# Kernel tuning notes

Measured on AMD Instinct MI355X. Metric: run time of the kernel, lower is better.

## Reference

```python
import jax, jax.numpy as jnp
from jax import lax
import numpy as np

B, P, S, K = 16, 4096, 1024, 16   # clouds, points/cloud, fps samples/cloud (ratio 0.25), knn k
IN_F, OUT_F = 256, 512
EPS = 1e-5


def setup_inputs() -> dict:
    key = jax.random.key(0)
    k1, k2, k3 = jax.random.split(key, 3)
    features = jax.random.normal(k1, (B * P, IN_F), jnp.float32)
    positions = jax.random.normal(k2, (B * P, 3), jnp.float32)
    batch = jnp.repeat(jnp.arange(B, dtype=jnp.int32), P)
    W = jax.random.normal(k3, (IN_F, OUT_F), jnp.float32) / np.sqrt(IN_F)
    b = jnp.zeros((OUT_F,), jnp.float32)
    gamma = jnp.ones((OUT_F,), jnp.float32)
    beta = jnp.zeros((OUT_F,), jnp.float32)
    return {"features": features, "positions": positions, "batch": batch,
            "W": W, "b": b, "gamma": gamma, "beta": beta}


def _fps_local(pos):
    """Farthest point sampling on one cloud. pos: [P,3] -> [S] int32 local indices.
    Deterministic start at index 0 (torch_cluster fps with random_start disabled)."""
    def step(carry, _):
        min_d, last = carry
        d = jnp.sum((pos - pos[last]) ** 2, axis=-1)
        min_d = jnp.minimum(min_d, d)
        nxt = jnp.argmax(min_d).astype(jnp.int32)
        return (min_d, nxt), last
    init = (jnp.full((pos.shape[0],), jnp.inf, pos.dtype), jnp.int32(0))
    _, idx = lax.scan(step, init, None, length=S)
    return idx


def _knn_local(q, x):
    """K nearest neighbors of queries q [S,F] among x [P,F] (squared L2). -> [S,K] int32."""
    d = jnp.sum(q * q, -1, keepdims=True) - 2.0 * (q @ x.T) + jnp.sum(x * x, -1)
    _, idx = lax.top_k(-d, K)
    return idx


def reference(features, positions, batch, W, b, gamma, beta):
    pos_b = positions.reshape(B, P, 3)
    feat_b = features.reshape(B, P, IN_F)

    # --- FPS on positions, per cloud ---
    fps_loc = jax.vmap(_fps_local)(pos_b)                      # [B,S]
    offsets = (jnp.arange(B, dtype=jnp.int32) * P)[:, None]    # [B,1]
    fps_glob = (fps_loc + offsets).reshape(-1)                 # [B*S]

    # --- MLP: Linear -> BatchNorm1d (training batch stats, biased var) -> ReLU ---
    h = features @ W + b                                       # [N,OUT_F]
    mu = jnp.mean(h, axis=0)
    var = jnp.var(h, axis=0)
    h = jax.nn.relu(gamma * (h - mu) * lax.rsqrt(var + EPS) + beta)

    # --- brute-force KNN in feature space: queries = features[fps_indices] ---
    q = jnp.take_along_axis(feat_b, fps_loc[..., None], axis=1)   # [B,S,IN_F]
    nn_loc = jax.vmap(_knn_local)(q, feat_b)                      # [B,S,K]
    nn_glob = nn_loc + offsets[..., None]                         # [B,S,K]

    # --- scatter max-pool: each query has exactly K neighbors -> max over K ---
    nb = h[nn_glob.reshape(-1)].reshape(B, S, K, OUT_F)
    new_features = jnp.max(nb, axis=2).reshape(B * S, OUT_F)

    return new_features, positions[fps_glob], batch[fps_glob]
```

## Files before the change

kernel.cpp:

```cpp
#include <hip/hip_runtime.h>
#include <cstddef>


#define TD_B   16
#define TD_P   4096
#define TD_S   1024
#define TD_K   16
#define TD_INF 256
#define TD_OUTF 512

typedef __attribute__((ext_vector_type(8))) _Float16 half8;
typedef __attribute__((ext_vector_type(4))) float    f32x4;
typedef __attribute__((ext_vector_type(2))) float    v2f;

__device__ __forceinline__ unsigned short f2bf(float x) {
    unsigned u = __float_as_uint(x);
    unsigned r = (u + 0x7fffu + ((u >> 16) & 1u)) >> 16;
    return (unsigned short)r;
}

struct FpsSm {
    float4 p4[TD_P];
    int    sel[TD_S];
    unsigned long long kw[2][8];
};
struct GemmSm {
    float As[16 * 260];
    float Bs[16 * 128];
};
union SmU {
    FpsSm f; GemmSm g;
    char pad_[84000];
};

#define TD_DPPSTEP(k, ctl, bc)                                                          \
    {                                                                                   \
        unsigned yh_ = (unsigned)__builtin_amdgcn_update_dpp(                           \
            0, (int)(unsigned)((k) >> 32), (ctl), 0xf, 0xf, (bc));                      \
        unsigned yl_ = (unsigned)__builtin_amdgcn_update_dpp(                           \
            0, (int)(unsigned)(k), (ctl), 0xf, 0xf, (bc));                              \
        unsigned long long y_ = ((unsigned long long)yh_ << 32) | yl_;                  \
        if (y_ > (k)) (k) = y_;                                                         \
    }

__global__ __launch_bounds__(512)
void td_fused(const float* __restrict__ feat, const float* __restrict__ pos,
              const float* __restrict__ W, const float* __restrict__ bias,
              unsigned short* __restrict__ H, float* __restrict__ XX,
              int* __restrict__ FPSI, float* __restrict__ outP,
              float* __restrict__ outB) {
    __shared__ SmU sm;
    const int bx = blockIdx.x;
    const int t  = threadIdx.x;

    if (bx < 16) {
        __builtin_amdgcn_s_setprio(2);
        const int b = bx;
        const int w = t >> 6;
        v2f px[8], py[8], pz[8], md[8];
        int ni0[8], ni1[8];
        float lx = 0.0f, ly = 0.0f, lz = 0.0f;
        if (t < 256) {
#pragma unroll
            for (int j = 0; j < 8; ++j) {
                int p0 = j * 512 + t, p1 = p0 + 256;
                const float* q0 = pos + (size_t)(b * TD_P + p0) * 3;
                const float* q1 = pos + (size_t)(b * TD_P + p1) * 3;
                float x0 = q0[0], y0 = q0[1], z0 = q0[2];
                float x1 = q1[0], y1 = q1[1], z1 = q1[2];
                px[j] = (v2f){x0, x1}; py[j] = (v2f){y0, y1}; pz[j] = (v2f){z0, z1};
                sm.f.p4[p0] = make_float4(x0, y0, z0, 0.0f);
                sm.f.p4[p1] = make_float4(x1, y1, z1, 0.0f);
                md[j] = (v2f){__builtin_inff(), __builtin_inff()};
                ni0[j] = ~p0; ni1[j] = ~p1;
            }
            if (t == 0) sm.f.sel[0] = 0;
        }
        __syncthreads();
        if (t < 256) { float4 wp = sm.f.p4[0]; lx = wp.x; ly = wp.y; lz = wp.z; }
        for (int s = 0; s < TD_S - 1; ++s) {
            const int par = s & 1;
            if (t < 256) {
                double k[16];
                {
#pragma clang fp contract(off)
                    v2f l2x = (v2f){lx, lx}, l2y = (v2f){ly, ly}, l2z = (v2f){lz, lz};
#pragma unroll
                    for (int j = 0; j < 8; ++j) {
                        v2f dx = px[j] - l2x;
                        v2f dy = py[j] - l2y;
                        v2f dz = pz[j] - l2z;
                        v2f sx = dx * dx;
                        v2f sy = dy * dy;
                        v2f sz = dz * dz;
                        v2f dd = (sx + sy) + sz;
                        md[j] = __builtin_elementwise_min(md[j], dd);
                        k[2 * j]     = __hiloint2double(__float_as_int(md[j].x), ni0[j]);
                        k[2 * j + 1] = __hiloint2double(__float_as_int(md[j].y), ni1[j]);
                    }
                }
#pragma unroll
                for (int st = 8; st > 0; st >>= 1)
#pragma unroll
                    for (int i = 0; i < st; ++i) k[i] = fmax(k[i], k[i + st]);
                unsigned long long tk = (unsigned long long)__double_as_longlong(k[0]);
                TD_DPPSTEP(tk, 0x111, true)
                TD_DPPSTEP(tk, 0x112, true)
                TD_DPPSTEP(tk, 0x114, true)
                TD_DPPSTEP(tk, 0x118, true)
                TD_DPPSTEP(tk, 0x142, false)
                TD_DPPSTEP(tk, 0x143, false)
                if ((t & 63) == 63) sm.f.kw[par][w] = tk;
            }
            __syncthreads();
            if (t < 256) {
                const unsigned long long* kwp = sm.f.kw[par];
                double g01 = fmax(__longlong_as_double((long long)kwp[0]),
                                  __longlong_as_double((long long)kwp[1]));
                double g23 = fmax(__longlong_as_double((long long)kwp[2]),
                                  __longlong_as_double((long long)kwp[3]));
                double gk  = fmax(g01, g23);
                unsigned idx = ~(unsigned)__double2loint(gk);
                if (t == 0) sm.f.sel[s + 1] = (int)idx;
                float4 wp = sm.f.p4[idx];
                lx = wp.x; ly = wp.y; lz = wp.z;
            }
        }
        __syncthreads();
        for (int s = t; s < TD_S; s += 512) {
            int li = sm.f.sel[s];
            int og = b * TD_S + s;
            float4 wp = sm.f.p4[li];
            outP[og * 3 + 0] = wp.x;
            outP[og * 3 + 1] = wp.y;
            outP[og * 3 + 2] = wp.z;
            outB[og] = (float)b;
            FPSI[og] = b * TD_P + li;
        }
    } else if (bx < 16 + 1024) {
        const int gb = bx - 16;
        const int mb = gb >> 2, nb = gb & 3;
        const int tm = t >> 4, tn = t & 15;
        float acc[8][8];
#pragma unroll
        for (int i = 0; i < 8; ++i)
#pragma unroll
            for (int j = 0; j < 8; ++j) acc[i][j] = 0.0f;
        float* As = sm.g.As;
        float* Bs = sm.g.Bs;
        for (int kc = 0; kc < 16; ++kc) {
#pragma unroll
            for (int p2 = 0; p2 < 2; ++p2) {
                int f4 = t + 512 * p2;
                int r = f4 >> 2, c4 = f4 & 3;
                float4 v = *(const float4*)&feat[(size_t)(mb * 256 + r) * 256 + kc * 16 + c4 * 4];
                As[(c4 * 4 + 0) * 260 + r] = v.x;
                As[(c4 * 4 + 1) * 260 + r] = v.y;
                As[(c4 * 4 + 2) * 260 + r] = v.z;
                As[(c4 * 4 + 3) * 260 + r] = v.w;
            }
            {
                int kk = t >> 5, n4 = t & 31;
                float4 v = *(const float4*)&W[(size_t)(kc * 16 + kk) * 512 + nb * 128 + n4 * 4];
                *(float4*)&Bs[kk * 128 + n4 * 4] = v;
            }
            __syncthreads();
#pragma unroll
            for (int kk = 0; kk < 16; ++kk) {
                float4 a0 = *(float4*)&As[kk * 260 + tm * 8];
                float4 a1 = *(float4*)&As[kk * 260 + tm * 8 + 4];
                float4 b0 = *(float4*)&Bs[kk * 128 + tn * 8];
                float4 b1 = *(float4*)&Bs[kk * 128 + tn * 8 + 4];
                float av[8] = {a0.x, a0.y, a0.z, a0.w, a1.x, a1.y, a1.z, a1.w};
                float bv2[8] = {b0.x, b0.y, b0.z, b0.w, b1.x, b1.y, b1.z, b1.w};
#pragma unroll
                for (int i = 0; i < 8; ++i)
#pragma unroll
                    for (int j = 0; j < 8; ++j)
                        acc[i][j] = fmaf(av[i], bv2[j], acc[i][j]);
            }
            __syncthreads();
        }
        float4 bb0 = *(const float4*)&bias[nb * 128 + tn * 8];
        float4 bb1 = *(const float4*)&bias[nb * 128 + tn * 8 + 4];
        float bsv[8] = {bb0.x, bb0.y, bb0.z, bb0.w, bb1.x, bb1.y, bb1.z, bb1.w};
#pragma unroll
        for (int i = 0; i < 8; ++i) {
            int row = mb * 256 + tm * 8 + i;
            uint4 pk;
            pk.x = (unsigned)f2bf(acc[i][0] + bsv[0]) | ((unsigned)f2bf(acc[i][1] + bsv[1]) << 16);
            pk.y = (unsigned)f2bf(acc[i][2] + bsv[2]) | ((unsigned)f2bf(acc[i][3] + bsv[3]) << 16);
            pk.z = (unsigned)f2bf(acc[i][4] + bsv[4]) | ((unsigned)f2bf(acc[i][5] + bsv[5]) << 16);
            pk.w = (unsigned)f2bf(acc[i][6] + bsv[6]) | ((unsigned)f2bf(acc[i][7] + bsv[7]) << 16);
            *(uint4*)&H[(size_t)row * 512 + nb * 128 + tn * 8] = pk;
        }
    } else {
        const int xb = bx - 1040;
        const int w = t >> 6, lane = t & 63;
#pragma unroll
        for (int it = 0; it < 8; ++it) {
            int r = xb * 64 + w * 8 + it;
            float4 v = *(const float4*)&feat[(size_t)r * 256 + lane * 4];
            float s = v.x * v.x + v.y * v.y + v.z * v.z + v.w * v.w;
#pragma unroll
            for (int off = 32; off > 0; off >>= 1) s += __shfl_down(s, off, 64);
            if (lane == 0) XX[r] = s;
        }
    }
}

__global__ __launch_bounds__(256)
void td_stats(const unsigned short* __restrict__ H, float* __restrict__ P1,
              float* __restrict__ P2) {
    const int rb = blockIdx.x, t = threadIdx.x;
    float s1a = 0, s2a = 0, s1b = 0, s2b = 0;
    for (int r = 0; r < 256; ++r) {
        const unsigned* hp = (const unsigned*)(H + (size_t)(rb * 256 + r) * 512);
        unsigned u = hp[t];
        float lo = __uint_as_float(u << 16);
        float hi = __uint_as_float(u & 0xffff0000u);
        s1a += lo; s2a = fmaf(lo, lo, s2a);
        s1b += hi; s2b = fmaf(hi, hi, s2b);
    }
    P1[rb * 512 + 2 * t] = s1a; P1[rb * 512 + 2 * t + 1] = s1b;
    P2[rb * 512 + 2 * t] = s2a; P2[rb * 512 + 2 * t + 1] = s2b;
}

__global__ __launch_bounds__(512)
void td_bnfin(const float* __restrict__ P1, const float* __restrict__ P2,
              const float* __restrict__ gamma, const float* __restrict__ beta,
              float* __restrict__ SS) {
    const int ch = threadIdx.x;
    float s1 = 0, s2 = 0;
    for (int rb = 0; rb < 256; ++rb) { s1 += P1[rb * 512 + ch]; s2 += P2[rb * 512 + ch]; }
    const float invN = 1.0f / 65536.0f;
    float mu  = s1 * invN;
    float var = s2 * invN - mu * mu;
    float sc  = gamma[ch] * (1.0f / sqrtf(var + 1e-5f));
    float sh  = beta[ch] - mu * sc;
    SS[ch] = sc; SS[512 + ch] = sh;
}

__global__ __launch_bounds__(256, 2)
void td_knn2(const float* __restrict__ feat, const float* __restrict__ XX,
             const int* __restrict__ FPSI, float* __restrict__ PD,
             int* __restrict__ PI) {
    __shared__ union {
        _Float16 x[2][32][264];
        float    dt[128][33];
    } sm;
    __shared__ float QQs[128];
    __shared__ int   QR[128];

    const int bx = blockIdx.x, t = threadIdx.x;
    const int b = bx & 15, r2 = bx >> 4;
    const int qq8 = r2 >> 2, seg = r2 & 3;
    const int cb = b * TD_P;
    const int segbase = cb + seg * 1024;

    if (t < 128) {
        int gr = FPSI[b * TD_S + qq8 * 128 + t];
        QR[t] = gr; QQs[t] = XX[gr];
    }
    __syncthreads();

    const int w = t >> 6, lane = t & 63;
    const int m = lane & 15, quad = lane >> 4;

    half8 qh[2][8], ql[2][8];
#pragma unroll
    for (int qs = 0; qs < 2; ++qs) {
        const float* qp = feat + (size_t)QR[w * 32 + qs * 16 + m] * 256;
#pragma unroll
        for (int ks = 0; ks < 8; ++ks) {
            float4 f0 = *(const float4*)(qp + ks * 32 + quad * 8);
            float4 f1 = *(const float4*)(qp + ks * 32 + quad * 8 + 4);
            float fv[8] = {f0.x, f0.y, f0.z, f0.w, f1.x, f1.y, f1.z, f1.w};
            half8 h, l;
#pragma unroll
            for (int j = 0; j < 8; ++j) {
                _Float16 hv = (_Float16)fv[j];
                h[j] = hv;
                l[j] = (_Float16)(fv[j] - (float)hv);
            }
            qh[qs][ks] = h; ql[qs][ks] = l;
        }
    }

    float sd[16]; int si[16];
#pragma unroll
    for (int r = 0; r < 16; ++r) { sd[r] = __builtin_inff(); si[r] = 0x7fffffff; }

    const int xrow = t >> 3, part = t & 7;

    for (int ct = 0; ct < 32; ++ct) {
        __syncthreads();
        {
            const float* xp = feat + (size_t)(segbase + ct * 32 + xrow) * 256 + part * 32;
#pragma unroll
            for (int s2 = 0; s2 < 4; ++s2) {
                float4 f0 = *(const float4*)(xp + s2 * 8);
                float4 f1 = *(const float4*)(xp + s2 * 8 + 4);
                float fv[8] = {f0.x, f0.y, f0.z, f0.w, f1.x, f1.y, f1.z, f1.w};
                half8 h, l;
#pragma unroll
                for (int j = 0; j < 8; ++j) {
                    _Float16 hv = (_Float16)fv[j];
                    h[j] = hv;
                    l[j] = (_Float16)(fv[j] - (float)hv);
                }
                *(half8*)&sm.x[0][xrow][part * 32 + s2 * 8] = h;
                *(half8*)&sm.x[1][xrow][part * 32 + s2 * 8] = l;
            }
        }
        __syncthreads();
        f32x4 acc[2][2];
        acc[0][0] = (f32x4)0.0f; acc[0][1] = (f32x4)0.0f;
        acc[1][0] = (f32x4)0.0f; acc[1][1] = (f32x4)0.0f;
#pragma unroll
        for (int ks = 0; ks < 8; ++ks) {
            half8 xh0 = *(half8*)&sm.x[0][m][ks * 32 + quad * 8];
            half8 xl0 = *(half8*)&sm.x[1][m][ks * 32 + quad * 8];
            half8 xh1 = *(half8*)&sm.x[0][16 + m][ks * 32 + quad * 8];
            half8 xl1 = *(half8*)&sm.x[1][16 + m][ks * 32 + quad * 8];
            acc[0][0] = __builtin_amdgcn_mfma_f32_16x16x32_f16(ql[0][ks], xh0, acc[0][0], 0, 0, 0);
            acc[0][1] = __builtin_amdgcn_mfma_f32_16x16x32_f16(ql[0][ks], xh1, acc[0][1], 0, 0, 0);
            acc[1][0] = __builtin_amdgcn_mfma_f32_16x16x32_f16(ql[1][ks], xh0, acc[1][0], 0, 0, 0);
            acc[1][1] = __builtin_amdgcn_mfma_f32_16x16x32_f16(ql[1][ks], xh1, acc[1][1], 0, 0, 0);
            acc[0][0] = __builtin_amdgcn_mfma_f32_16x16x32_f16(qh[0][ks], xl0, acc[0][0], 0, 0, 0);
            acc[0][1] = __builtin_amdgcn_mfma_f32_16x16x32_f16(qh[0][ks], xl1, acc[0][1], 0, 0, 0);
            acc[1][0] = __builtin_amdgcn_mfma_f32_16x16x32_f16(qh[1][ks], xl0, acc[1][0], 0, 0, 0);
            acc[1][1] = __builtin_amdgcn_mfma_f32_16x16x32_f16(qh[1][ks], xl1, acc[1][1], 0, 0, 0);
            acc[0][0] = __builtin_amdgcn_mfma_f32_16x16x32_f16(qh[0][ks], xh0, acc[0][0], 0, 0, 0);
            acc[0][1] = __builtin_amdgcn_mfma_f32_16x16x32_f16(qh[0][ks], xh1, acc[0][1], 0, 0, 0);
            acc[1][0] = __builtin_amdgcn_mfma_f32_16x16x32_f16(qh[1][ks], xh0, acc[1][0], 0, 0, 0);
            acc[1][1] = __builtin_amdgcn_mfma_f32_16x16x32_f16(qh[1][ks], xh1, acc[1][1], 0, 0, 0);
        }
        __syncthreads();
        {
            float xx0 = XX[segbase + ct * 32 + m];
            float xx1 = XX[segbase + ct * 32 + 16 + m];
#pragma unroll
            for (int qs = 0; qs < 2; ++qs) {
                int qb = w * 32 + qs * 16 + quad * 4;
#pragma unroll
                for (int reg = 0; reg < 4; ++reg) {
                    float qq = QQs[qb + reg];
                    sm.dt[qb + reg][m]      = (qq - 2.0f * acc[qs][0][reg]) + xx0;
                    sm.dt[qb + reg][16 + m] = (qq - 2.0f * acc[qs][1][reg]) + xx1;
                }
            }
        }
        __syncthreads();
        if (t < 128) {
            const int ibase = segbase + ct * 32;
            for (int j = 0; j < 32; ++j) {
                float d = sm.dt[t][j];
                if (d < sd[15]) {
                    sd[15] = d; si[15] = ibase + j;
#pragma unroll
                    for (int r = 15; r > 0; --r) {
                        if (sd[r] < sd[r - 1]) {
                            float td2 = sd[r]; sd[r] = sd[r - 1]; sd[r - 1] = td2;
                            int ti = si[r]; si[r] = si[r - 1]; si[r - 1] = ti;
                        }
                    }
                }
            }
        }
    }
    if (t < 128) {
        size_t o = ((size_t)(b * TD_S + qq8 * 128 + t)) * 64 + seg * 16;
#pragma unroll
        for (int r = 0; r < 16; ++r) { PD[o + r] = sd[r]; PI[o + r] = si[r]; }
    }
}

__global__ __launch_bounds__(64)
void td_merge(const float* __restrict__ PD, const int* __restrict__ PI,
              int* __restrict__ NN) {
    __shared__ float ld_[64][65];
    __shared__ int   li_[64][65];
    const int bx = blockIdx.x, t = threadIdx.x;
    for (int j = 0; j < 64; ++j) {
        ld_[j][t] = PD[(size_t)bx * 4096 + j * 64 + t];
        li_[j][t] = PI[(size_t)bx * 4096 + j * 64 + t];
    }
    __syncthreads();
    int p[4] = {0, 0, 0, 0};
    int og = (bx * 64 + t) * TD_K;
    for (int r = 0; r < 16; ++r) {
        float bd = __builtin_inff(); int bi = 0x7fffffff; int bs = 0;
#pragma unroll
        for (int s = 0; s < 4; ++s) {
            if (p[s] < 16) {
                float d = ld_[t][s * 16 + p[s]];
                int   i = li_[t][s * 16 + p[s]];
                if (d < bd || (d == bd && i < bi)) { bd = d; bi = i; bs = s; }
            }
        }
        p[bs]++;
        NN[og + r] = bi;
    }
}

__global__ __launch_bounds__(256)
void td_maxpool(const unsigned short* __restrict__ H, const int* __restrict__ NN,
                const float* __restrict__ SS, float* __restrict__ outF) {
    __shared__ int nbr[64];
    const int bx = blockIdx.x, t = threadIdx.x;
    const int cloud = bx & 15, blk = bx >> 4;
    const int qbase = cloud * 1024 + blk * 4;
    if (t < 64) nbr[t] = NN[(size_t)qbase * 16 + t];
    __syncthreads();
    float sc0 = SS[2 * t], sc1 = SS[2 * t + 1];
    float sh0 = SS[512 + 2 * t], sh1 = SS[512 + 2 * t + 1];
#pragma unroll
    for (int qi = 0; qi < 4; ++qi) {
        float m0 = 0.0f, m1 = 0.0f;
#pragma unroll
        for (int k = 0; k < 16; ++k) {
            int row = nbr[qi * 16 + k];
            unsigned u = ((const unsigned*)(H + (size_t)row * 512))[t];
            float lo = __uint_as_float(u << 16);
            float hi = __uint_as_float(u & 0xffff0000u);
            m0 = fmaxf(m0, fmaf(sc0, lo, sh0));
            m1 = fmaxf(m1, fmaf(sc1, hi, sh1));
        }
        float2 o; o.x = m0; o.y = m1;
        *(float2*)&outF[(size_t)(qbase + qi) * 512 + 2 * t] = o;
    }
}

extern "C" void kernel_launch(void* const* d_in, const int* in_sizes, int n_in,
                              void* d_out, int out_size, void* d_ws, size_t ws_size,
                              hipStream_t stream) {
    const float* feat  = (const float*)d_in[0];
    const float* pos   = (const float*)d_in[1];
    const float* W     = (const float*)d_in[3];
    const float* bias  = (const float*)d_in[4];
    const float* gamma = (const float*)d_in[5];
    const float* beta  = (const float*)d_in[6];

    char* ws = (char*)d_ws;
    unsigned short* H = (unsigned short*)ws;
    float* XX  = (float*)(ws + 67108864);
    int*   FPSI= (int*)  (ws + 67371008);
    int*   NN  = (int*)  (ws + 67436544);
    float* P1  = (float*)(ws + 68485120);
    float* P2  = (float*)(ws + 69533696);
    float* SS  = (float*)(ws + 70582272);
    float* PD  = (float*)(ws + 70586368);
    int*   PI  = (int*)  (ws + 74780672);

    float* outF = (float*)d_out;
    float* outP = outF + (size_t)TD_B * TD_S * TD_OUTF;
    float* outB = outP + (size_t)TD_B * TD_S * 3;

    td_fused  <<<2064, 512, 0, stream>>>(feat, pos, W, bias, H, XX, FPSI, outP, outB);
    td_stats  <<<256, 256, 0, stream>>>(H, P1, P2);
    td_bnfin  <<<1, 512, 0, stream>>>(P1, P2, gamma, beta, SS);
    td_knn2   <<<512, 256, 0, stream>>>(feat, XX, FPSI, PD, PI);
    td_merge  <<<256, 64, 0, stream>>>(PD, PI, NN);
    td_maxpool<<<TD_B * 256, 256, 0, stream>>>(H, NN, SS, outF);
}
```

Before: 1.102 ms.

## Fuse all stages into one persistent kernel with flag-based inter-block dependencies

Merges the GEMM, BN stats, BN finalize, KNN, merge and maxpool kernels into a single launch. Blocks wait on acquire/release flags in global memory, so KNN on early FPS samples can start while FPS is still running, and maxpool runs as each merge group finishes. Row norms are now computed inside the KNN tiles instead of a separate XX pass, and the DPP argmax reduction works on doubles with fmax. This removes launch gaps and serialisation but depends on blocks being scheduled in index order, which risks deadlock or stalls from spinning blocks holding CU slots.

```diff
diff --git a/kernel.cpp b/kernel.cpp
--- a/kernel.cpp
+++ b/kernel.cpp
@@ -19,36 +19,63 @@
     return (unsigned short)r;
 }
 
+__device__ __forceinline__ int ld_acq(const int* p) {
+    return __hip_atomic_load(p, __ATOMIC_ACQUIRE, __HIP_MEMORY_SCOPE_AGENT);
+}
+__device__ __forceinline__ void st_rel(int* p, int v) {
+    __hip_atomic_store(p, v, __ATOMIC_RELEASE, __HIP_MEMORY_SCOPE_AGENT);
+}
+__device__ __forceinline__ void add_rel(int* p, int v) {
+    __hip_atomic_fetch_add(p, v, __ATOMIC_RELEASE, __HIP_MEMORY_SCOPE_AGENT);
+}
+
 struct FpsSm {
     float4 p4[TD_P];
     int    sel[TD_S];
-    unsigned long long kw[2][8];
+    unsigned long long kw[2][4];
 };
 struct GemmSm {
     float As[16 * 260];
     float Bs[16 * 128];
 };
+struct KnnSm {
+    union {
+        _Float16 x[2][32][264];
+        float    dt[256][33];
+    } u;
+    float QQs[256];
+    int   QR[256];
+    float xxs[32];
+};
+struct MergeSm {
+    float ld[64][130];
+    int   li[64][130];
+};
+struct MaxpSm { int nbr[128]; };
 union SmU {
-    FpsSm f; GemmSm g;
+    FpsSm f; GemmSm g; KnnSm k; MergeSm m; MaxpSm mp;
     char pad_[84000];
 };
 
-#define TD_DPPSTEP(k, ctl, bc)                                                          \
+#define TD_DPPSTEPD(kd_, ctl, bc)                                                       \
     {                                                                                   \
+        long long ki_ = __double_as_longlong(kd_);                                      \
         unsigned yh_ = (unsigned)__builtin_amdgcn_update_dpp(                           \
-            0, (int)(unsigned)((k) >> 32), (ctl), 0xf, 0xf, (bc));                      \
+            0, (int)((unsigned long long)ki_ >> 32), (ctl), 0xf, 0xf, (bc));            \
         unsigned yl_ = (unsigned)__builtin_amdgcn_update_dpp(                           \
-            0, (int)(unsigned)(k), (ctl), 0xf, 0xf, (bc));                              \
-        unsigned long long y_ = ((unsigned long long)yh_ << 32) | yl_;                  \
-        if (y_ > (k)) (k) = y_;                                                         \
+            0, (int)(unsigned)(unsigned long long)ki_, (ctl), 0xf, 0xf, (bc));          \
+        kd_ = fmax(kd_, __hiloint2double((int)yh_, (int)yl_));                          \
     }
 
 __global__ __launch_bounds__(512)
-void td_fused(const float* __restrict__ feat, const float* __restrict__ pos,
-              const float* __restrict__ W, const float* __restrict__ bias,
-              unsigned short* __restrict__ H, float* __restrict__ XX,
-              int* __restrict__ FPSI, float* __restrict__ outP,
-              float* __restrict__ outB) {
+void td_all(const float* __restrict__ feat, const float* __restrict__ pos,
+            const float* __restrict__ W, const float* __restrict__ bias,
+            const float* __restrict__ gamma, const float* __restrict__ beta,
+            unsigned short* __restrict__ H, int* __restrict__ FPSI,
+            int* __restrict__ NN, float* __restrict__ P1, float* __restrict__ P2,
+            float* __restrict__ SS, float* __restrict__ PD, int* __restrict__ PI,
+            float* __restrict__ outF, float* __restrict__ outP,
+            float* __restrict__ outB, int* __restrict__ flags) {
     __shared__ SmU sm;
     const int bx = blockIdx.x;
     const int t  = threadIdx.x;
@@ -103,27 +130,33 @@
                 for (int st = 8; st > 0; st >>= 1)
 #pragma unroll
                     for (int i = 0; i < st; ++i) k[i] = fmax(k[i], k[i + st]);
-                unsigned long long tk = (unsigned long long)__double_as_longlong(k[0]);
-                TD_DPPSTEP(tk, 0x111, true)
-                TD_DPPSTEP(tk, 0x112, true)
-                TD_DPPSTEP(tk, 0x114, true)
-                TD_DPPSTEP(tk, 0x118, true)
-                TD_DPPSTEP(tk, 0x142, false)
-                TD_DPPSTEP(tk, 0x143, false)
-                if ((t & 63) == 63) sm.f.kw[par][w] = tk;
+                double tk = k[0];
+                TD_DPPSTEPD(tk, 0x111, true)
+                TD_DPPSTEPD(tk, 0x112, true)
+                TD_DPPSTEPD(tk, 0x114, true)
+                TD_DPPSTEPD(tk, 0x118, true)
+                TD_DPPSTEPD(tk, 0x142, false)
+                TD_DPPSTEPD(tk, 0x143, false)
+                if ((t & 63) == 63)
+                    sm.f.kw[par][w] = (unsigned long long)__double_as_longlong(tk);
             }
             __syncthreads();
             if (t < 256) {
-                const unsigned long long* kwp = sm.f.kw[par];
-                double g01 = fmax(__longlong_as_double((long long)kwp[0]),
-                                  __longlong_as_double((long long)kwp[1]));
-                double g23 = fmax(__longlong_as_double((long long)kwp[2]),
-                                  __longlong_as_double((long long)kwp[3]));
-                double gk  = fmax(g01, g23);
+                const double2* kd = (const double2*)sm.f.kw[par];
+                double2 va = kd[0], vb = kd[1];
+                double gk = fmax(fmax(va.x, va.y), fmax(vb.x, vb.y));
                 unsigned idx = ~(unsigned)__double2loint(gk);
                 if (t == 0) sm.f.sel[s + 1] = (int)idx;
                 float4 wp = sm.f.p4[idx];
                 lx = wp.x; ly = wp.y; lz = wp.z;
+            }
+            if (t < 64 && (s & 127) == 127 && s < 896) {
+                int c = s >> 7;
+                int i0 = c * 128 + 2 * t;
+                FPSI[b * TD_S + i0]     = b * TD_P + sm.f.sel[i0];
+                FPSI[b * TD_S + i0 + 1] = b * TD_P + sm.f.sel[i0 + 1];
+                __threadfence();
+                if (t == 0) st_rel(flags + b, c + 1);
             }
         }
         __syncthreads();
@@ -137,6 +170,8 @@
             outB[og] = (float)b;
             FPSI[og] = b * TD_P + li;
         }
+        __syncthreads();
+        if (t == 0) { __threadfence(); st_rel(flags + b, 8); }
     } else if (bx < 16 + 1024) {
         const int gb = bx - 16;
         const int mb = gb >> 2, nb = gb & 3;
@@ -194,113 +229,33 @@
             pk.w = (unsigned)f2bf(acc[i][6] + bsv[6]) | ((unsigned)f2bf(acc[i][7] + bsv[7]) << 16);
             *(uint4*)&H[(size_t)row * 512 + nb * 128 + tn * 8] = pk;
         }
-    } else {
-        const int xb = bx - 1040;
+        __syncthreads();
+        if (t == 0) { __threadfence(); add_rel(flags + 16, 1); }
+    } else if (bx < 1552) {
+        const int kb = bx - 1040;
+        const int b = kb & 15, r2 = kb >> 4;
+        const int qqp = r2 >> 3, seg = r2 & 7;
+        const int segbase = b * TD_P + seg * 512;
+        const int qbase = b * TD_S + qqp * 256;
+        if (t == 0) {
+            while (ld_acq(flags + b) < 2 * qqp + 2) __builtin_amdgcn_s_sleep(16);
+        }
+        __syncthreads();
+        if (t < 256) sm.k.QR[t] = FPSI[qbase + t];
+        __syncthreads();
+
         const int w = t >> 6, lane = t & 63;
-#pragma unroll
-        for (int it = 0; it < 8; ++it) {
-            int r = xb * 64 + w * 8 + it;
-            float4 v = *(const float4*)&feat[(size_t)r * 256 + lane * 4];
-            float s = v.x * v.x + v.y * v.y + v.z * v.z + v.w * v.w;
-#pragma unroll
-            for (int off = 32; off > 0; off >>= 1) s += __shfl_down(s, off, 64);
-            if (lane == 0) XX[r] = s;
-        }
-    }
-}
-
-__global__ __launch_bounds__(256)
-void td_stats(const unsigned short* __restrict__ H, float* __restrict__ P1,
-              float* __restrict__ P2) {
-    const int rb = blockIdx.x, t = threadIdx.x;
-    float s1a = 0, s2a = 0, s1b = 0, s2b = 0;
-    for (int r = 0; r < 256; ++r) {
-        const unsigned* hp = (const unsigned*)(H + (size_t)(rb * 256 + r) * 512);
-        unsigned u = hp[t];
-        float lo = __uint_as_float(u << 16);
-        float hi = __uint_as_float(u & 0xffff0000u);
-        s1a += lo; s2a = fmaf(lo, lo, s2a);
-        s1b += hi; s2b = fmaf(hi, hi, s2b);
-    }
-    P1[rb * 512 + 2 * t] = s1a; P1[rb * 512 + 2 * t + 1] = s1b;
-    P2[rb * 512 + 2 * t] = s2a; P2[rb * 512 + 2 * t + 1] = s2b;
-}
-
-__global__ __launch_bounds__(512)
-void td_bnfin(const float* __restrict__ P1, const float* __restrict__ P2,
-              const float* __restrict__ gamma, const float* __restrict__ beta,
-              float* __restrict__ SS) {
-    const int ch = threadIdx.x;
-    float s1 = 0, s2 = 0;
-    for (int rb = 0; rb < 256; ++rb) { s1 += P1[rb * 512 + ch]; s2 += P2[rb * 512 + ch]; }
-    const float invN = 1.0f / 65536.0f;
-    float mu  = s1 * invN;
-    float var = s2 * invN - mu * mu;
-    float sc  = gamma[ch] * (1.0f / sqrtf(var + 1e-5f));
-    float sh  = beta[ch] - mu * sc;
-    SS[ch] = sc; SS[512 + ch] = sh;
-}
-
-__global__ __launch_bounds__(256, 2)
-void td_knn2(const float* __restrict__ feat, const float* __restrict__ XX,
-             const int* __restrict__ FPSI, float* __restrict__ PD,
-             int* __restrict__ PI) {
-    __shared__ union {
-        _Float16 x[2][32][264];
-        float    dt[128][33];
-    } sm;
-    __shared__ float QQs[128];
-    __shared__ int   QR[128];
-
-    const int bx = blockIdx.x, t = threadIdx.x;
-    const int b = bx & 15, r2 = bx >> 4;
-    const int qq8 = r2 >> 2, seg = r2 & 3;
-    const int cb = b * TD_P;
-    const int segbase = cb + seg * 1024;
-
-    if (t < 128) {
-        int gr = FPSI[b * TD_S + qq8 * 128 + t];
-        QR[t] = gr; QQs[t] = XX[gr];
-    }
-    __syncthreads();
-
-    const int w = t >> 6, lane = t & 63;
-    const int m = lane & 15, quad = lane >> 4;
-
-    half8 qh[2][8], ql[2][8];
-#pragma unroll
-    for (int qs = 0; qs < 2; ++qs) {
-        const float* qp = feat + (size_t)QR[w * 32 + qs * 16 + m] * 256;
-#pragma unroll
-        for (int ks = 0; ks < 8; ++ks) {
-            float4 f0 = *(const float4*)(qp + ks * 32 + quad * 8);
-            float4 f1 = *(const float4*)(qp + ks * 32 + quad * 8 + 4);
-            float fv[8] = {f0.x, f0.y, f0.z, f0.w, f1.x, f1.y, f1.z, f1.w};
-            half8 h, l;
-#pragma unroll
-            for (int j = 0; j < 8; ++j) {
-                _Float16 hv = (_Float16)fv[j];
-                h[j] = hv;
-                l[j] = (_Float16)(fv[j] - (float)hv);
-            }
-            qh[qs][ks] = h; ql[qs][ks] = l;
-        }
-    }
-
-    float sd[16]; int si[16];
-#pragma unroll
-    for (int r = 0; r < 16; ++r) { sd[r] = __builtin_inff(); si[r] = 0x7fffffff; }
-
-    const int xrow = t >> 3, part = t & 7;
-
-    for (int ct = 0; ct < 32; ++ct) {
-        __syncthreads();
-        {
-            const float* xp = feat + (size_t)(segbase + ct * 32 + xrow) * 256 + part * 32;
-#pragma unroll
-            for (int s2 = 0; s2 < 4; ++s2) {
-                float4 f0 = *(const float4*)(xp + s2 * 8);
-                float4 f1 = *(const float4*)(xp + s2 * 8 + 4);
+        const int m = lane & 15, quad = lane >> 4;
+
+        half8 qh[2][8], ql[2][8];
+#pragma unroll
+        for (int qs = 0; qs < 2; ++qs) {
+            const float* qp = feat + (size_t)sm.k.QR[w * 32 + qs * 16 + m] * 256;
+            float qq2 = 0.0f;
+#pragma unroll
+            for (int ks = 0; ks < 8; ++ks) {
+                float4 f0 = *(const float4*)(qp + ks * 32 + quad * 8);
+                float4 f1 = *(const float4*)(qp + ks * 32 + quad * 8 + 4);
                 float fv[8] = {f0.x, f0.y, f0.z, f0.w, f1.x, f1.y, f1.z, f1.w};
                 half8 h, l;
 #pragma unroll
@@ -308,56 +263,181 @@
                     _Float16 hv = (_Float16)fv[j];
                     h[j] = hv;
                     l[j] = (_Float16)(fv[j] - (float)hv);
-                }
-                *(half8*)&sm.x[0][xrow][part * 32 + s2 * 8] = h;
-                *(half8*)&sm.x[1][xrow][part * 32 + s2 * 8] = l;
-            }
-        }
-        __syncthreads();
-        f32x4 acc[2][2];
-        acc[0][0] = (f32x4)0.0f; acc[0][1] = (f32x4)0.0f;
-        acc[1][0] = (f32x4)0.0f; acc[1][1] = (f32x4)0.0f;
-#pragma unroll
-        for (int ks = 0; ks < 8; ++ks) {
-            half8 xh0 = *(half8*)&sm.x[0][m][ks * 32 + quad * 8];
-            half8 xl0 = *(half8*)&sm.x[1][m][ks * 32 + quad * 8];
-            half8 xh1 = *(half8*)&sm.x[0][16 + m][ks * 32 + quad * 8];
-            half8 xl1 = *(half8*)&sm.x[1][16 + m][ks * 32 + quad * 8];
-            acc[0][0] = __builtin_amdgcn_mfma_f32_16x16x32_f16(ql[0][ks], xh0, acc[0][0], 0, 0, 0);
-            acc[0][1] = __builtin_amdgcn_mfma_f32_16x16x32_f16(ql[0][ks], xh1, acc[0][1], 0, 0, 0);
-            acc[1][0] = __builtin_amdgcn_mfma_f32_16x16x32_f16(ql[1][ks], xh0, acc[1][0], 0, 0, 0);
-            acc[1][1] = __builtin_amdgcn_mfma_f32_16x16x32_f16(ql[1][ks], xh1, acc[1][1], 0, 0, 0);
-            acc[0][0] = __builtin_amdgcn_mfma_f32_16x16x32_f16(qh[0][ks], xl0, acc[0][0], 0, 0, 0);
-            acc[0][1] = __builtin_amdgcn_mfma_f32_16x16x32_f16(qh[0][ks], xl1, acc[0][1], 0, 0, 0);
-            acc[1][0] = __builtin_amdgcn_mfma_f32_16x16x32_f16(qh[1][ks], xl0, acc[1][0], 0, 0, 0);
-            acc[1][1] = __builtin_amdgcn_mfma_f32_16x16x32_f16(qh[1][ks], xl1, acc[1][1], 0, 0, 0);
-            acc[0][0] = __builtin_amdgcn_mfma_f32_16x16x32_f16(qh[0][ks], xh0, acc[0][0], 0, 0, 0);
-            acc[0][1] = __builtin_amdgcn_mfma_f32_16x16x32_f16(qh[0][ks], xh1, acc[0][1], 0, 0, 0);
-            acc[1][0] = __builtin_amdgcn_mfma_f32_16x16x32_f16(qh[1][ks], xh0, acc[1][0], 0, 0, 0);
-            acc[1][1] = __builtin_amdgcn_mfma_f32_16x16x32_f16(qh[1][ks], xh1, acc[1][1], 0, 0, 0);
+                    qq2 = fmaf(fv[j], fv[j], qq2);
+                }
+                qh[qs][ks] = h; ql[qs][ks] = l;
+            }
+            qq2 += __shfl_xor(qq2, 16, 64);
+            qq2 += __shfl_xor(qq2, 32, 64);
+            if (quad == 0) sm.k.QQs[w * 32 + qs * 16 + m] = qq2;
+        }
+
+        float sd[16]; int si[16];
+#pragma unroll
+        for (int r = 0; r < 16; ++r) { sd[r] = __builtin_inff(); si[r] = 0x7fffffff; }
+
+        const int xrow = t >> 4, part = t & 15;
+
+        for (int ct = 0; ct < 16; ++ct) {
+            __syncthreads();
+            {
+                const float* xp = feat + (size_t)(segbase + ct * 32 + xrow) * 256 + part * 16;
+                float4 f0 = *(const float4*)(xp);
+                float4 f1 = *(const float4*)(xp + 4);
+                float4 f2 = *(const float4*)(xp + 8);
+                float4 f3 = *(const float4*)(xp + 12);
+                float fv[16] = {f0.x, f0.y, f0.z, f0.w, f1.x, f1.y, f1.z, f1.w,
+                                f2.x, f2.y, f2.z, f2.w, f3.x, f3.y, f3.z, f3.w};
+                half8 h0, h1, l0, l1;
+                float cn = 0.0f;
+#pragma unroll
+                for (int j = 0; j < 8; ++j) {
+                    _Float16 hv = (_Float16)fv[j];
+                    h0[j] = hv; l0[j] = (_Float16)(fv[j] - (float)hv);
+                    cn = fmaf(fv[j], fv[j], cn);
+                }
+#pragma unroll
+                for (int j = 0; j < 8; ++j) {
+                    float v = fv[8 + j];
+                    _Float16 hv = (_Float16)v;
+                    h1[j] = hv; l1[j] = (_Float16)(v - (float)hv);
+                    cn = fmaf(v, v, cn);
+                }
+                *(half8*)&sm.k.u.x[0][xrow][part * 16]     = h0;
+                *(half8*)&sm.k.u.x[0][xrow][part * 16 + 8] = h1;
+                *(half8*)&sm.k.u.x[1][xrow][part * 16]     = l0;
+                *(half8*)&sm.k.u.x[1][xrow][part * 16 + 8] = l1;
+                cn += __shfl_xor(cn, 1, 64);
+                cn += __shfl_xor(cn, 2, 64);
+                cn += __shfl_xor(cn, 4, 64);
+                cn += __shfl_xor(cn, 8, 64);
+                if (part == 0) sm.k.xxs[xrow] = cn;
+            }
+            __syncthreads();
+            f32x4 acc[2][2];
+            acc[0][0] = (f32x4)0.0f; acc[0][1] = (f32x4)0.0f;
+            acc[1][0] = (f32x4)0.0f; acc[1][1] = (f32x4)0.0f;
+#pragma unroll
+            for (int ks = 0; ks < 8; ++ks) {
+                half8 xh0 = *(half8*)&sm.k.u.x[0][m][ks * 32 + quad * 8];
+                half8 xl0 = *(half8*)&sm.k.u.x[1][m][ks * 32 + quad * 8];
+                half8 xh1 = *(half8*)&sm.k.u.x[0][16 + m][ks * 32 + quad * 8];
+                half8 xl1 = *(half8*)&sm.k.u.x[1][16 + m][ks * 32 + quad * 8];
+                acc[0][0] = __builtin_amdgcn_mfma_f32_16x16x32_f16(ql[0][ks], xh0, acc[0][0], 0, 0, 0);
+                acc[0][1] = __builtin_amdgcn_mfma_f32_16x16x32_f16(ql[0][ks], xh1, acc[0][1], 0, 0, 0);
+                acc[1][0] = __builtin_amdgcn_mfma_f32_16x16x32_f16(ql[1][ks], xh0, acc[1][0], 0, 0, 0);
+                acc[1][1] = __builtin_amdgcn_mfma_f32_16x16x32_f16(ql[1][ks], xh1, acc[1][1], 0, 0, 0);
+                acc[0][0] = __builtin_amdgcn_mfma_f32_16x16x32_f16(qh[0][ks], xl0, acc[0][0], 0, 0, 0);
+                acc[0][1] = __builtin_amdgcn_mfma_f32_16x16x32_f16(qh[0][ks], xl1, acc[0][1], 0, 0, 0);
+                acc[1][0] = __builtin_amdgcn_mfma_f32_16x16x32_f16(qh[1][ks], xl0, acc[1][0], 0, 0, 0);
+                acc[1][1] = __builtin_amdgcn_mfma_f32_16x16x32_f16(qh[1][ks], xl1, acc[1][1], 0, 0, 0);
+                acc[0][0] = __builtin_amdgcn_mfma_f32_16x16x32_f16(qh[0][ks], xh0, acc[0][0], 0, 0, 0);
+                acc[0][1] = __builtin_amdgcn_mfma_f32_16x16x32_f16(qh[0][ks], xh1, acc[0][1], 0, 0, 0);
+                acc[1][0] = __builtin_amdgcn_mfma_f32_16x16x32_f16(qh[1][ks], xh0, acc[1][0], 0, 0, 0);
+                acc[1][1] = __builtin_amdgcn_mfma_f32_16x16x32_f16(qh[1][ks], xh1, acc[1][1], 0, 0, 0);
+            }
+            __syncthreads();
+            {
+                float xx0 = sm.k.xxs[m];
+                float xx1 = sm.k.xxs[16 + m];
+#pragma unroll
+                for (int qs = 0; qs < 2; ++qs) {
+                    int qb = w * 32 + qs * 16 + quad * 4;
+#pragma unroll
+                    for (int reg = 0; reg < 4; ++reg) {
+                        float qq = sm.k.QQs[qb + reg];
+                        sm.k.u.dt[qb + reg][m]      = (qq - 2.0f * acc[qs][0][reg]) + xx0;
+                        sm.k.u.dt[qb + reg][16 + m] = (qq - 2.0f * acc[qs][1][reg]) + xx1;
+                    }
+                }
+            }
+            __syncthreads();
+            if (t < 256) {
+                const int ibase = segbase + ct * 32;
+                for (int j = 0; j < 32; ++j) {
+                    float d = sm.k.u.dt[t][j];
+                    if (d < sd[15]) {
+                        sd[15] = d; si[15] = ibase + j;
+#pragma unroll
+                        for (int r = 15; r > 0; --r) {
+                            if (sd[r] < sd[r - 1]) {
+                                float td2 = sd[r]; sd[r] = sd[r - 1]; sd[r - 1] = td2;
+                                int ti = si[r]; si[r] = si[r - 1]; si[r - 1] = ti;
+                            }
+                        }
+                    }
+                }
+            }
+        }
+        if (t < 256) {
+            size_t o = ((size_t)(qbase + t)) * 128 + seg * 16;
+#pragma unroll
+            for (int r = 0; r < 16; ++r) { PD[o + r] = sd[r]; PI[o + r] = si[r]; }
+        }
+        __syncthreads();
+        if (t == 0) { __threadfence(); add_rel(flags + 24 + b * 4 + qqp, 1); }
+    } else if (bx < 1808) {
+        const int rb = bx - 1552;
+        if (t == 0) {
+            while (ld_acq(flags + 16) < 1024) __builtin_amdgcn_s_sleep(32);
+        }
+        __syncthreads();
+        if (t < 256) {
+            float s1a = 0, s2a = 0, s1b = 0, s2b = 0;
+            for (int r = 0; r < 256; ++r) {
+                const unsigned* hp = (const unsigned*)(H + (size_t)(rb * 256 + r) * 512);
+                unsigned u = hp[t];
+                float lo = __uint_as_float(u << 16);
+                float hi = __uint_as_float(u & 0xffff0000u);
+                s1a += lo; s2a = fmaf(lo, lo, s2a);
+                s1b += hi; s2b = fmaf(hi, hi, s2b);
+            }
+            P1[rb * 512 + 2 * t] = s1a; P1[rb * 512 + 2 * t + 1] = s1b;
+            P2[rb * 512 + 2 * t] = s2a; P2[rb * 512 + 2 * t + 1] = s2b;
+        }
+        __syncthreads();
+        if (t == 0) { __threadfence(); add_rel(flags + 17, 1); }
+    } else if (bx == 1808) {
+        if (t == 0) {
+            while (ld_acq(flags + 17) < 256) __builtin_amdgcn_s_sleep(32);
         }
         __syncthreads();
         {
-            float xx0 = XX[segbase + ct * 32 + m];
-            float xx1 = XX[segbase + ct * 32 + 16 + m];
-#pragma unroll
-            for (int qs = 0; qs < 2; ++qs) {
-                int qb = w * 32 + qs * 16 + quad * 4;
-#pragma unroll
-                for (int reg = 0; reg < 4; ++reg) {
-                    float qq = QQs[qb + reg];
-                    sm.dt[qb + reg][m]      = (qq - 2.0f * acc[qs][0][reg]) + xx0;
-                    sm.dt[qb + reg][16 + m] = (qq - 2.0f * acc[qs][1][reg]) + xx1;
-                }
-            }
-        }
-        __syncthreads();
-        if (t < 128) {
-            const int ibase = segbase + ct * 32;
-            for (int j = 0; j < 32; ++j) {
-                float d = sm.dt[t][j];
+            const int ch = t;
+            float s1 = 0, s2 = 0;
+            for (int rb2 = 0; rb2 < 256; ++rb2) {
+                s1 += P1[rb2 * 512 + ch]; s2 += P2[rb2 * 512 + ch];
+            }
+            const float invN = 1.0f / 65536.0f;
+            float mu  = s1 * invN;
+            float var = s2 * invN - mu * mu;
+            float sc  = gamma[ch] * (1.0f / sqrtf(var + 1e-5f));
+            float sh  = beta[ch] - mu * sc;
+            SS[ch] = sc; SS[512 + ch] = sh;
+        }
+        __syncthreads();
+        if (t == 0) { __threadfence(); st_rel(flags + 18, 1); }
+    } else if (bx < 2065) {
+        const int mb = bx - 1809;
+        const int cloud = mb >> 4, qqp = (mb >> 2) & 3;
+        if (t == 0) {
+            while (ld_acq(flags + 24 + cloud * 4 + qqp) < 8) __builtin_amdgcn_s_sleep(16);
+        }
+        __syncthreads();
+        for (int i = t; i < 64 * 128; i += 512) {
+            int qi = i >> 7, j = i & 127;
+            sm.m.ld[qi][j] = PD[(size_t)mb * 8192 + i];
+            sm.m.li[qi][j] = PI[(size_t)mb * 8192 + i];
+        }
+        __syncthreads();
+        if (t < 64) {
+            float sd[16]; int si[16];
+#pragma unroll
+            for (int r = 0; r < 16; ++r) { sd[r] = __builtin_inff(); si[r] = 0x7fffffff; }
+            for (int j = 0; j < 128; ++j) {
+                float d = sm.m.ld[t][j];
                 if (d < sd[15]) {
-                    sd[15] = d; si[15] = ibase + j;
+                    sd[15] = d; si[15] = sm.m.li[t][j];
 #pragma unroll
                     for (int r = 15; r > 0; --r) {
                         if (sd[r] < sd[r - 1]) {
@@ -367,68 +447,42 @@
                     }
                 }
             }
-        }
-    }
-    if (t < 128) {
-        size_t o = ((size_t)(b * TD_S + qq8 * 128 + t)) * 64 + seg * 16;
-#pragma unroll
-        for (int r = 0; r < 16; ++r) { PD[o + r] = sd[r]; PI[o + r] = si[r]; }
-    }
-}
-
-__global__ __launch_bounds__(64)
-void td_merge(const float* __restrict__ PD, const int* __restrict__ PI,
-              int* __restrict__ NN) {
-    __shared__ float ld_[64][65];
-    __shared__ int   li_[64][65];
-    const int bx = blockIdx.x, t = threadIdx.x;
-    for (int j = 0; j < 64; ++j) {
-        ld_[j][t] = PD[(size_t)bx * 4096 + j * 64 + t];
-        li_[j][t] = PI[(size_t)bx * 4096 + j * 64 + t];
-    }
-    __syncthreads();
-    int p[4] = {0, 0, 0, 0};
-    int og = (bx * 64 + t) * TD_K;
-    for (int r = 0; r < 16; ++r) {
-        float bd = __builtin_inff(); int bi = 0x7fffffff; int bs = 0;
-#pragma unroll
-        for (int s = 0; s < 4; ++s) {
-            if (p[s] < 16) {
-                float d = ld_[t][s * 16 + p[s]];
-                int   i = li_[t][s * 16 + p[s]];
-                if (d < bd || (d == bd && i < bi)) { bd = d; bi = i; bs = s; }
-            }
-        }
-        p[bs]++;
-        NN[og + r] = bi;
-    }
-}
-
-__global__ __launch_bounds__(256)
-void td_maxpool(const unsigned short* __restrict__ H, const int* __restrict__ NN,
-                const float* __restrict__ SS, float* __restrict__ outF) {
-    __shared__ int nbr[64];
-    const int bx = blockIdx.x, t = threadIdx.x;
-    const int cloud = bx & 15, blk = bx >> 4;
-    const int qbase = cloud * 1024 + blk * 4;
-    if (t < 64) nbr[t] = NN[(size_t)qbase * 16 + t];
-    __syncthreads();
-    float sc0 = SS[2 * t], sc1 = SS[2 * t + 1];
-    float sh0 = SS[512 + 2 * t], sh1 = SS[512 + 2 * t + 1];
-#pragma unroll
-    for (int qi = 0; qi < 4; ++qi) {
-        float m0 = 0.0f, m1 = 0.0f;
-#pragma unroll
-        for (int k = 0; k < 16; ++k) {
-            int row = nbr[qi * 16 + k];
-            unsigned u = ((const unsigned*)(H + (size_t)row * 512))[t];
-            float lo = __uint_as_float(u << 16);
-            float hi = __uint_as_float(u & 0xffff0000u);
-            m0 = fmaxf(m0, fmaf(sc0, lo, sh0));
-            m1 = fmaxf(m1, fmaf(sc1, hi, sh1));
-        }
-        float2 o; o.x = m0; o.y = m1;
-        *(float2*)&outF[(size_t)(qbase + qi) * 512 + 2 * t] = o;
+            int og = (mb * 64 + t) * TD_K;
+#pragma unroll
+            for (int r = 0; r < 16; ++r) NN[og + r] = si[r];
+        }
+        __syncthreads();
+        if (t == 0) { __threadfence(); st_rel(flags + 96 + mb, 1); }
+    } else {
+        const int pb = bx - 2065;
+        const int qbase8 = pb * 8;
+        const int mrg = qbase8 >> 6;
+        if (t == 0) {
+            while (ld_acq(flags + 96 + mrg) == 0) __builtin_amdgcn_s_sleep(16);
+            while (ld_acq(flags + 18) == 0) __builtin_amdgcn_s_sleep(16);
+        }
+        __syncthreads();
+        if (t < 128) sm.mp.nbr[t] = NN[(size_t)qbase8 * 16 + t];
+        __syncthreads();
+        const int hq = t >> 8, tc = t & 255;
+        float sc0 = SS[2 * tc], sc1 = SS[2 * tc + 1];
+        float sh0 = SS[512 + 2 * tc], sh1 = SS[512 + 2 * tc + 1];
+#pragma unroll
+        for (int qi = 0; qi < 4; ++qi) {
+            const int q = hq * 4 + qi;
+            float m0 = 0.0f, m1 = 0.0f;
+#pragma unroll
+            for (int k = 0; k < 16; ++k) {
+                int row = sm.mp.nbr[q * 16 + k];
+                unsigned u = ((const unsigned*)(H + (size_t)row * 512))[tc];
+                float lo = __uint_as_float(u << 16);
+                float hi = __uint_as_float(u & 0xffff0000u);
+                m0 = fmaxf(m0, fmaf(sc0, lo, sh0));
+                m1 = fmaxf(m1, fmaf(sc1, hi, sh1));
+            }
+            float2 o; o.x = m0; o.y = m1;
+            *(float2*)&outF[(size_t)(qbase8 + q) * 512 + 2 * tc] = o;
+        }
     }
 }
 
@@ -443,24 +497,22 @@
     const float* beta  = (const float*)d_in[6];
 
     char* ws = (char*)d_ws;
-    unsigned short* H = (unsigned short*)ws;
-    float* XX  = (float*)(ws + 67108864);
-    int*   FPSI= (int*)  (ws + 67371008);
-    int*   NN  = (int*)  (ws + 67436544);
-    float* P1  = (float*)(ws + 68485120);
-    float* P2  = (float*)(ws + 69533696);
-    float* SS  = (float*)(ws + 70582272);
-    float* PD  = (float*)(ws + 70586368);
-    int*   PI  = (int*)  (ws + 74780672);
+    int* flags        = (int*)ws;
+    unsigned short* H = (unsigned short*)(ws + 4096);
+    int*   FPSI = (int*)  (ws + 67112960);
+    int*   NN   = (int*)  (ws + 67178496);
+    float* P1   = (float*)(ws + 68227072);
+    float* P2   = (float*)(ws + 68751360);
+    float* SS   = (float*)(ws + 69275648);
+    float* PD   = (float*)(ws + 69279744);
+    int*   PI   = (int*)  (ws + 77668352);
 
     float* outF = (float*)d_out;
     float* outP = outF + (size_t)TD_B * TD_S * TD_OUTF;
     float* outB = outP + (size_t)TD_B * TD_S * 3;
 
-    td_fused  <<<2064, 512, 0, stream>>>(feat, pos, W, bias, H, XX, FPSI, outP, outB);
-    td_stats  <<<256, 256, 0, stream>>>(H, P1, P2);
-    td_bnfin  <<<1, 512, 0, stream>>>(P1, P2, gamma, beta, SS);
-    td_knn2   <<<512, 256, 0, stream>>>(feat, XX, FPSI, PD, PI);
-    td_merge  <<<256, 64, 0, stream>>>(PD, PI, NN);
-    td_maxpool<<<TD_B * 256, 256, 0, stream>>>(H, NN, SS, outF);
+    hipMemsetAsync(flags, 0, 2048, stream);
+    td_all<<<4113, 512, 0, stream>>>(feat, pos, W, bias, gamma, beta,
+                                     H, FPSI, NN, P1, P2, SS, PD, PI,
+                                     outF, outP, outB, flags);
 }
```

Measured after the change: 1.181 ms. 1.07x slower.

## Fuse BN statistics into GEMM epilogue and compute squared norms inside KNN

Applied to the files above, without the earlier changes.

Batch-norm sum and sum-of-squares are now accumulated in the GEMM epilogue from fp32 values and reduced per block through shared memory. This removes the separate td_stats kernel that re-read the bf16 H buffer. The XX row-norm blocks are dropped from the fused kernel, and the KNN kernel computes query and candidate squared norms on the fly while converting features. This removes one launch and a pass over H, at the cost of extra FMAs, shuffles and syncs. The statistics now come from unrounded fp32 values instead of bf16, which changes the numerics slightly.

```diff
diff --git a/kernel.cpp b/kernel.cpp
--- a/kernel.cpp
+++ b/kernel.cpp
@@ -46,9 +46,9 @@
 __global__ __launch_bounds__(512)
 void td_fused(const float* __restrict__ feat, const float* __restrict__ pos,
               const float* __restrict__ W, const float* __restrict__ bias,
-              unsigned short* __restrict__ H, float* __restrict__ XX,
-              int* __restrict__ FPSI, float* __restrict__ outP,
-              float* __restrict__ outB) {
+              unsigned short* __restrict__ H, int* __restrict__ FPSI,
+              float* __restrict__ outP, float* __restrict__ outB,
+              float* __restrict__ P1p, float* __restrict__ P2p) {
     __shared__ SmU sm;
     const int bx = blockIdx.x;
     const int t  = threadIdx.x;
@@ -137,7 +137,7 @@
             outB[og] = (float)b;
             FPSI[og] = b * TD_P + li;
         }
-    } else if (bx < 16 + 1024) {
+    } else {
         const int gb = bx - 16;
         const int mb = gb >> 2, nb = gb & 3;
         const int tm = t >> 4, tn = t & 15;
@@ -184,55 +184,57 @@
         float4 bb0 = *(const float4*)&bias[nb * 128 + tn * 8];
         float4 bb1 = *(const float4*)&bias[nb * 128 + tn * 8 + 4];
         float bsv[8] = {bb0.x, bb0.y, bb0.z, bb0.w, bb1.x, bb1.y, bb1.z, bb1.w};
+        float s1v[8], s2v[8];
+#pragma unroll
+        for (int j = 0; j < 8; ++j) { s1v[j] = 0.0f; s2v[j] = 0.0f; }
 #pragma unroll
         for (int i = 0; i < 8; ++i) {
             int row = mb * 256 + tm * 8 + i;
+            float hh[8];
+#pragma unroll
+            for (int j = 0; j < 8; ++j) {
+                hh[j] = acc[i][j] + bsv[j];
+                s1v[j] += hh[j];
+                s2v[j] = fmaf(hh[j], hh[j], s2v[j]);
+            }
             uint4 pk;
-            pk.x = (unsigned)f2bf(acc[i][0] + bsv[0]) | ((unsigned)f2bf(acc[i][1] + bsv[1]) << 16);
-            pk.y = (unsigned)f2bf(acc[i][2] + bsv[2]) | ((unsigned)f2bf(acc[i][3] + bsv[3]) << 16);
-            pk.z = (unsigned)f2bf(acc[i][4] + bsv[4]) | ((unsigned)f2bf(acc[i][5] + bsv[5]) << 16);
-            pk.w = (unsigned)f2bf(acc[i][6] + bsv[6]) | ((unsigned)f2bf(acc[i][7] + bsv[7]) << 16);
+            pk.x = (unsigned)f2bf(hh[0]) | ((unsigned)f2bf(hh[1]) << 16);
+            pk.y = (unsigned)f2bf(hh[2]) | ((unsigned)f2bf(hh[3]) << 16);
+            pk.z = (unsigned)f2bf(hh[4]) | ((unsigned)f2bf(hh[5]) << 16);
+            pk.w = (unsigned)f2bf(hh[6]) | ((unsigned)f2bf(hh[7]) << 16);
             *(uint4*)&H[(size_t)row * 512 + nb * 128 + tn * 8] = pk;
         }
-    } else {
-        const int xb = bx - 1040;
-        const int w = t >> 6, lane = t & 63;
-#pragma unroll
-        for (int it = 0; it < 8; ++it) {
-            int r = xb * 64 + w * 8 + it;
-            float4 v = *(const float4*)&feat[(size_t)r * 256 + lane * 4];
-            float s = v.x * v.x + v.y * v.y + v.z * v.z + v.w * v.w;
-#pragma unroll
-            for (int off = 32; off > 0; off >>= 1) s += __shfl_down(s, off, 64);
-            if (lane == 0) XX[r] = s;
-        }
-    }
-}
-
-__global__ __launch_bounds__(256)
-void td_stats(const unsigned short* __restrict__ H, float* __restrict__ P1,
-              float* __restrict__ P2) {
-    const int rb = blockIdx.x, t = threadIdx.x;
-    float s1a = 0, s2a = 0, s1b = 0, s2b = 0;
-    for (int r = 0; r < 256; ++r) {
-        const unsigned* hp = (const unsigned*)(H + (size_t)(rb * 256 + r) * 512);
-        unsigned u = hp[t];
-        float lo = __uint_as_float(u << 16);
-        float hi = __uint_as_float(u & 0xffff0000u);
-        s1a += lo; s2a = fmaf(lo, lo, s2a);
-        s1b += hi; s2b = fmaf(hi, hi, s2b);
-    }
-    P1[rb * 512 + 2 * t] = s1a; P1[rb * 512 + 2 * t + 1] = s1b;
-    P2[rb * 512 + 2 * t] = s2a; P2[rb * 512 + 2 * t + 1] = s2b;
+        float* red = As;
+#pragma unroll
+        for (int j = 0; j < 8; ++j) red[tm * 128 + tn * 8 + j] = s1v[j];
+        __syncthreads();
+        float r1 = 0.0f;
+        if (t < 128) {
+            for (int r = 0; r < 32; ++r) r1 += red[r * 128 + t];
+        }
+        __syncthreads();
+#pragma unroll
+        for (int j = 0; j < 8; ++j) red[tm * 128 + tn * 8 + j] = s2v[j];
+        __syncthreads();
+        if (t < 128) {
+            float r2 = 0.0f;
+            for (int r = 0; r < 32; ++r) r2 += red[r * 128 + t];
+            P1p[mb * 512 + nb * 128 + t] = r1;
+            P2p[mb * 512 + nb * 128 + t] = r2;
+        }
+    }
 }
 
 __global__ __launch_bounds__(512)
-void td_bnfin(const float* __restrict__ P1, const float* __restrict__ P2,
+void td_bnfin(const float* __restrict__ P1p, const float* __restrict__ P2p,
               const float* __restrict__ gamma, const float* __restrict__ beta,
               float* __restrict__ SS) {
     const int ch = threadIdx.x;
     float s1 = 0, s2 = 0;
-    for (int rb = 0; rb < 256; ++rb) { s1 += P1[rb * 512 + ch]; s2 += P2[rb * 512 + ch]; }
+    for (int mb = 0; mb < 256; ++mb) {
+        s1 += P1p[mb * 512 + ch];
+        s2 += P2p[mb * 512 + ch];
+    }
     const float invN = 1.0f / 65536.0f;
     float mu  = s1 * invN;
     float var = s2 * invN - mu * mu;
@@ -242,26 +244,22 @@
 }
 
 __global__ __launch_bounds__(256, 2)
-void td_knn2(const float* __restrict__ feat, const float* __restrict__ XX,
-             const int* __restrict__ FPSI, float* __restrict__ PD,
-             int* __restrict__ PI) {
+void td_knn2(const float* __restrict__ feat, const int* __restrict__ FPSI,
+             float* __restrict__ PD, int* __restrict__ PI) {
     __shared__ union {
         _Float16 x[2][32][264];
         float    dt[128][33];
     } sm;
     __shared__ float QQs[128];
     __shared__ int   QR[128];
+    __shared__ float xxs[32];
 
     const int bx = blockIdx.x, t = threadIdx.x;
     const int b = bx & 15, r2 = bx >> 4;
     const int qq8 = r2 >> 2, seg = r2 & 3;
-    const int cb = b * TD_P;
-    const int segbase = cb + seg * 1024;
-
-    if (t < 128) {
-        int gr = FPSI[b * TD_S + qq8 * 128 + t];
-        QR[t] = gr; QQs[t] = XX[gr];
-    }
+    const int segbase = b * TD_P + seg * 1024;
+
+    if (t < 128) QR[t] = FPSI[b * TD_S + qq8 * 128 + t];
     __syncthreads();
 
     const int w = t >> 6, lane = t & 63;
@@ -271,6 +269,7 @@
 #pragma unroll
     for (int qs = 0; qs < 2; ++qs) {
         const float* qp = feat + (size_t)QR[w * 32 + qs * 16 + m] * 256;
+        float qq2 = 0.0f;
 #pragma unroll
         for (int ks = 0; ks < 8; ++ks) {
             float4 f0 = *(const float4*)(qp + ks * 32 + quad * 8);
@@ -282,9 +281,13 @@
                 _Float16 hv = (_Float16)fv[j];
                 h[j] = hv;
                 l[j] = (_Float16)(fv[j] - (float)hv);
+                qq2 = fmaf(fv[j], fv[j], qq2);
             }
             qh[qs][ks] = h; ql[qs][ks] = l;
         }
+        qq2 += __shfl_xor(qq2, 16, 64);
+        qq2 += __shfl_xor(qq2, 32, 64);
+        if (quad == 0) QQs[w * 32 + qs * 16 + m] = qq2;
     }
 
     float sd[16]; int si[16];
@@ -297,6 +300,7 @@
         __syncthreads();
         {
             const float* xp = feat + (size_t)(segbase + ct * 32 + xrow) * 256 + part * 32;
+            float cn = 0.0f;
 #pragma unroll
             for (int s2 = 0; s2 < 4; ++s2) {
                 float4 f0 = *(const float4*)(xp + s2 * 8);
@@ -308,10 +312,15 @@
                     _Float16 hv = (_Float16)fv[j];
                     h[j] = hv;
                     l[j] = (_Float16)(fv[j] - (float)hv);
+                    cn = fmaf(fv[j], fv[j], cn);
                 }
                 *(half8*)&sm.x[0][xrow][part * 32 + s2 * 8] = h;
                 *(half8*)&sm.x[1][xrow][part * 32 + s2 * 8] = l;
             }
+            cn += __shfl_xor(cn, 1, 64);
+            cn += __shfl_xor(cn, 2, 64);
+            cn += __shfl_xor(cn, 4, 64);
+            if (part == 0) xxs[xrow] = cn;
         }
         __syncthreads();
         f32x4 acc[2][2];
@@ -338,8 +347,8 @@
         }
         __syncthreads();
         {
-            float xx0 = XX[segbase + ct * 32 + m];
-            float xx1 = XX[segbase + ct * 32 + 16 + m];
+            float xx0 = xxs[m];
+            float xx1 = xxs[16 + m];
 #pragma unroll
             for (int qs = 0; qs < 2; ++qs) {
                 int qb = w * 32 + qs * 16 + quad * 4;
@@ -444,23 +453,21 @@
 
     char* ws = (char*)d_ws;
     unsigned short* H = (unsigned short*)ws;
-    float* XX  = (float*)(ws + 67108864);
-    int*   FPSI= (int*)  (ws + 67371008);
-    int*   NN  = (int*)  (ws + 67436544);
-    float* P1  = (float*)(ws + 68485120);
-    float* P2  = (float*)(ws + 69533696);
-    float* SS  = (float*)(ws + 70582272);
-    float* PD  = (float*)(ws + 70586368);
-    int*   PI  = (int*)  (ws + 74780672);
+    int*   FPSI= (int*)  (ws + 67108864);
+    int*   NN  = (int*)  (ws + 67174400);
+    float* P1p = (float*)(ws + 68222976);
+    float* P2p = (float*)(ws + 68747264);
+    float* SS  = (float*)(ws + 69271552);
+    float* PD  = (float*)(ws + 69275648);
+    int*   PI  = (int*)  (ws + 73469952);
 
     float* outF = (float*)d_out;
     float* outP = outF + (size_t)TD_B * TD_S * TD_OUTF;
     float* outB = outP + (size_t)TD_B * TD_S * 3;
 
-    td_fused  <<<2064, 512, 0, stream>>>(feat, pos, W, bias, H, XX, FPSI, outP, outB);
-    td_stats  <<<256, 256, 0, stream>>>(H, P1, P2);
-    td_bnfin  <<<1, 512, 0, stream>>>(P1, P2, gamma, beta, SS);
-    td_knn2   <<<512, 256, 0, stream>>>(feat, XX, FPSI, PD, PI);
+    td_fused  <<<1040, 512, 0, stream>>>(feat, pos, W, bias, H, FPSI, outP, outB, P1p, P2p);
+    td_bnfin  <<<1, 512, 0, stream>>>(P1p, P2p, gamma, beta, SS);
+    td_knn2   <<<512, 256, 0, stream>>>(feat, FPSI, PD, PI);
     td_merge  <<<256, 64, 0, stream>>>(PD, PI, NN);
     td_maxpool<<<TD_B * 256, 256, 0, stream>>>(H, NN, SS, outF);
 }
```

Result: no change. 1.081 ms (-1.9%).
